# Performance work log

Measured on AMD Instinct MI355X. Metric: run time of the kernel, lower is better.

Reference implementation:

```python
import jax, jax.numpy as jnp
import numpy as np

EPS_BN = 1e-5
CLAMP_MAX = 1e-10  # nn.Hardtanh(min_val=0, max_val=1e-10) on squared dists


def _three_nn(xyz1, xyz2):
    # xyz1: (b, n, 3), xyz2: (b, m, 3) -> sq dists (b, n, 3), idx (b, n, 3)
    d2 = (jnp.sum(xyz1 ** 2, -1, keepdims=True)
          - 2.0 * jnp.einsum('bnc,bmc->bnm', xyz1, xyz2)
          + jnp.sum(xyz2 ** 2, -1)[:, None, :])  # (b, n, m)
    neg, idx = jax.lax.top_k(-d2, 3)
    return -neg, idx


def _conv_bn_relu(x, W, b, g, beta):
    # x: (b, n, cin); 1x1 Conv2d == pointwise linear, BN over (batch, spatial)
    y = jnp.einsum('bnc,oc->bno', x, W) + b
    mean = jnp.mean(y, axis=(0, 1))
    var = jnp.mean((y - mean) ** 2, axis=(0, 1))
    y = (y - mean) * jax.lax.rsqrt(var + EPS_BN) * g + beta
    return jax.nn.relu(y)


def setup_inputs() -> dict:
    key = jax.random.key(0)
    ks = jax.random.split(key, 8)
    b, n, m, c1, c2 = 16, 4096, 1024, 256, 512
    mlp, dimin = [256, 256], [c1 + c2, 256]
    inp = {
        'xyz1': jax.random.normal(ks[0], (b, n, 3), jnp.float32),
        'xyz2': jax.random.normal(ks[1], (b, m, 3), jnp.float32),
        'points1': jax.random.normal(ks[2], (b, n, c1), jnp.float32),
        'points2': jax.random.normal(ks[3], (b, m, c2), jnp.float32),
        'W1': jax.random.normal(ks[4], (mlp[0], dimin[0]), jnp.float32) * 0.02,
        'b1': jnp.zeros((mlp[0],), jnp.float32),
        'g1': jnp.ones((mlp[0],), jnp.float32),
        'beta1': jnp.zeros((mlp[0],), jnp.float32),
        'W2': jax.random.normal(ks[5], (mlp[1], dimin[1]), jnp.float32) * 0.02,
        'b2': jnp.zeros((mlp[1],), jnp.float32),
        'g2': jnp.ones((mlp[1],), jnp.float32),
        'beta2': jnp.zeros((mlp[1],), jnp.float32),
    }
    return inp


def reference(xyz1, xyz2, points1, points2, W1, b1, g1, beta1, W2, b2, g2, beta2):
    dist, idx = _three_nn(xyz1, xyz2)                     # (b, n, 3)
    dist = jnp.clip(dist, 0.0, CLAMP_MAX)                 # Hardtanh(0, 1e-10)
    inv = 1.0 / dist
    weight = inv / jnp.sum(inv, axis=2, keepdims=True)    # (b, n, 3)
    neigh = jax.vmap(lambda p, i: p[i])(points2, idx)     # (b, n, 3, c2)
    interp = jnp.einsum('bnk,bnkc->bnc', weight, neigh)   # (b, n, c2)
    feat = jnp.concatenate([interp, points1], axis=2)     # (b, n, c2+c1)
    feat = _conv_bn_relu(feat, W1, b1, g1, beta1)
    feat = _conv_bn_relu(feat, W2, b2, g2, beta2)
    return jnp.transpose(feat, (0, 2, 1))                 # (b, c_out, n)
```

## Files before the change

### kernel.cpp

```cpp
#include <hip/hip_runtime.h>

typedef unsigned short u16;
typedef short sh8 __attribute__((ext_vector_type(8)));
typedef float floatx4 __attribute__((ext_vector_type(4)));
typedef float float4v __attribute__((ext_vector_type(4)));
typedef u16 us8 __attribute__((ext_vector_type(8)));
typedef u16 us4 __attribute__((ext_vector_type(4)));

#define NB    16
#define NPTS  4096
#define MPTS  1024
#define CC1   256
#define CC2   512
#define KK1   768
#define CCO   256
#define MT    (NB*NPTS)
#define MZ    (NB*MPTS)

__device__ __forceinline__ float b2f(u16 u) {
    union { unsigned i; float f; } v; v.i = ((unsigned)u) << 16; return v.f;
}
__device__ __forceinline__ u16 f2b(float f) {
    union { float f; unsigned i; } v; v.f = f;
    unsigned u = v.i;
    unsigned r = (u + 0x7fffu + ((u >> 16) & 1u)) >> 16;
    return (u16)r;
}
__device__ __forceinline__ float ldv(const void* p, size_t i, int f32) {
    return f32 ? ((const float*)p)[i] : b2f(((const u16*)p)[i]);
}
__device__ __forceinline__ void stv(void* p, size_t i, int f32, float v) {
    if (f32) ((float*)p)[i] = v; else ((u16*)p)[i] = f2b(v);
}
__device__ __forceinline__ void gl_lds16(const void* g, void* l) {
    __builtin_amdgcn_global_load_lds(
        (const __attribute__((address_space(1))) void*)g,
        (__attribute__((address_space(3))) void*)l, 16, 0, 0);
}

__global__ void Pointnet_fp_module_33071248179394_kernel(
        const unsigned* g1bits, int* flag, float* stats) {
    int i = blockIdx.x * 256 + threadIdx.x;
    stats[i] = 0.f;
    if (i == 0) flag[0] = (g1bits[0] == 0x3F800000u) ? 1 : 0;
}

__global__ __launch_bounds__(512) void three_nn_k(
        const int* flagp, const void* xyz1, const void* xyz2,
        int* nidx, float* nw) {
    __shared__ float4 P[MPTS];
    __shared__ float md[512][3];
    __shared__ int   mi[512][3];
    const int f32 = flagp[0];
    const int bi = blockIdx.x >> 6;
    const int chunk = blockIdx.x & 63;
    const int t = threadIdx.x;
    const int ql = t & 63, sp = t >> 6;

    for (int p = t; p < MPTS; p += 512) {
        size_t s = (size_t)(bi * MPTS + p) * 3;
        P[p] = make_float4(ldv(xyz2, s, f32), ldv(xyz2, s + 1, f32),
                           ldv(xyz2, s + 2, f32), 0.f);
    }
    __syncthreads();

    const int q = chunk * 64 + ql;
    size_t s1 = (size_t)(bi * NPTS + q) * 3;
    const float qx = ldv(xyz1, s1 + 0, f32);
    const float qy = ldv(xyz1, s1 + 1, f32);
    const float qz = ldv(xyz1, s1 + 2, f32);

    float d0 = 3e38f, d1 = 3e38f, dv2 = 3e38f;
    int i0 = -1, i1 = -1, i2 = -1;
    const int jbeg = sp * 128, jend = jbeg + 128;
    #pragma unroll 4
    for (int j = jbeg; j < jend; j++) {
        float4 p = P[j];
        float dx = qx - p.x;
        float dy = qy - p.y;
        float dz = qz - p.z;
        float dd = fmaf(dx, dx, fmaf(dy, dy, dz * dz));
        if (dd < dv2) {
            if (dd < d0)      { dv2 = d1; i2 = i1; d1 = d0; i1 = i0; d0 = dd; i0 = j; }
            else if (dd < d1) { dv2 = d1; i2 = i1; d1 = dd; i1 = j; }
            else              { dv2 = dd; i2 = j; }
        }
    }
    md[t][0] = d0;  md[t][1] = d1;  md[t][2] = dv2;
    mi[t][0] = i0;  mi[t][1] = i1;  mi[t][2] = i2;
    __syncthreads();

    if (t < 64) {
        float b0 = 3e38f, b1 = 3e38f, b2v = 3e38f;
        int j0 = -1, j1 = -1, j2 = -1;
        #pragma unroll
        for (int s = 0; s < 8; s++) {
            int base = s * 64 + t;
            #pragma unroll
            for (int k = 0; k < 3; k++) {
                float d = md[base][k];
                int ji = mi[base][k];
                if (d < b0)      { b2v = b1; j2 = j1; b1 = b0; j1 = j0; b0 = d; j0 = ji; }
                else if (d < b1) { b2v = b1; j2 = j1; b1 = d; j1 = ji; }
                else if (d < b2v){ b2v = d; j2 = ji; }
            }
        }
        float e0 = fminf(fmaxf(b0, 0.f), 1e-10f);
        float e1 = fminf(fmaxf(b1, 0.f), 1e-10f);
        float e2 = fminf(fmaxf(b2v, 0.f), 1e-10f);
        float v0 = 1.0f / e0, v1 = 1.0f / e1, v2 = 1.0f / e2;
        float s = v0 + v1 + v2;
        const size_t gq = ((size_t)bi * NPTS + chunk * 64 + t) * 3;
        nidx[gq + 0] = j0; nidx[gq + 1] = j1; nidx[gq + 2] = j2;
        nw[gq + 0] = v0 / s; nw[gq + 1] = v1 / s; nw[gq + 2] = v2 / s;
    }
}

__global__ __launch_bounds__(256) void cvt_w_k(
        const int* flagp, const void* W1, const void* W2,
        u16* Wa, u16* Wbp, u16* W2b) {
    const int f32 = flagp[0];
    const int i = blockIdx.x * 256 + threadIdx.x;
    if (i < CCO * CC2) {
        int r = i >> 9, c = i & 511;
        Wa[i] = f2b(ldv(W1, (size_t)r * KK1 + c, f32));
    } else if (i < CCO * CC2 + CCO * CC1) {
        int k = i - CCO * CC2;
        int r = k >> 8, c = k & 255;
        Wbp[k] = f2b(ldv(W1, (size_t)r * KK1 + CC2 + c, f32));
    } else {
        int k = i - CCO * CC2 - CCO * CC1;
        W2b[k] = f2b(ldv(W2, k, f32));
    }
}

__global__ __launch_bounds__(256) void cvt_pts_k(
        const int* flagp, const void* p2, const void* p1,
        u16* p2b, u16* p1b) {
    const int f32 = flagp[0];
    size_t i = ((size_t)blockIdx.x * 256 + threadIdx.x) * 8;
    const size_t N2 = (size_t)MZ * CC2;
    const void* src; u16* dst; size_t off;
    if (i < N2) { src = p2; dst = p2b; off = i; }
    else        { src = p1; dst = p1b; off = i - N2; }
    us8 o;
    if (f32) {
        float4v a = *(const float4v*)((const float*)src + off);
        float4v b = *(const float4v*)((const float*)src + off + 4);
        #pragma unroll
        for (int k = 0; k < 4; k++) { o[k] = f2b(a[k]); o[k + 4] = f2b(b[k]); }
    } else {
        o = *(const us8*)((const u16*)src + off);
    }
    *(us8*)(dst + off) = o;
}

template<int K, bool STATS>
__global__ __launch_bounds__(256, 2) void gemm_bt(
        const int* flagp, const u16* __restrict__ A, const u16* __restrict__ B,
        const void* __restrict__ bias, u16* __restrict__ Y,
        float* __restrict__ sum, float* __restrict__ sq) {
    __shared__ u16 As[128 * 32];
    __shared__ u16 Bs[128 * 32];
    __shared__ float sSum[128], sSq[128];
    const int f32 = flagp[0];
    const int tid = threadIdx.x;
    const int m0 = blockIdx.x * 128;
    const int n0 = blockIdx.y * 128;
    const int wave = tid >> 6, lane = tid & 63;
    const int wm = wave & 1, wn = wave >> 1;
    const int l16 = lane & 15, quad = lane >> 4;

    if (STATS && tid < 128) { sSum[tid] = 0.f; sSq[tid] = 0.f; }

    floatx4 acc[4][4];
    #pragma unroll
    for (int i = 0; i < 4; i++)
        #pragma unroll
        for (int j = 0; j < 4; j++)
            acc[i][j] = (floatx4){0.f, 0.f, 0.f, 0.f};

    for (int kb = 0; kb < K; kb += 32) {
        __syncthreads();
        #pragma unroll
        for (int tt = 0; tt < 2; tt++) {
            int chunk = tid + tt * 256;
            int row = chunk >> 2, c4 = chunk & 3;
            gl_lds16(A + (size_t)(m0 + row) * K + kb + c4 * 8, As + chunk * 8);
            gl_lds16(B + (size_t)(n0 + row) * K + kb + c4 * 8, Bs + chunk * 8);
        }
        __syncthreads();

        sh8 af[4], bfr[4];
        #pragma unroll
        for (int i = 0; i < 4; i++)
            af[i] = *(const sh8*)(As + (wm * 64 + i * 16 + l16) * 32 + quad * 8);
        #pragma unroll
        for (int j = 0; j < 4; j++)
            bfr[j] = *(const sh8*)(Bs + (wn * 64 + j * 16 + l16) * 32 + quad * 8);
        #pragma unroll
        for (int i = 0; i < 4; i++)
            #pragma unroll
            for (int j = 0; j < 4; j++)
                acc[i][j] = __builtin_amdgcn_mfma_f32_16x16x32_bf16(
                                bfr[j], af[i], acc[i][j], 0, 0, 0);
    }

    float bvv[4][4];
    #pragma unroll
    for (int j = 0; j < 4; j++)
        #pragma unroll
        for (int r = 0; r < 4; r++) {
            int col = n0 + wn * 64 + j * 16 + quad * 4 + r;
            bvv[j][r] = bias ? ldv(bias, col, f32) : 0.f;
        }

    float cs[4][4], css[4][4];
    if (STATS) {
        #pragma unroll
        for (int j = 0; j < 4; j++)
            #pragma unroll
            for (int r = 0; r < 4; r++) { cs[j][r] = 0.f; css[j][r] = 0.f; }
    }

    #pragma unroll
    for (int i = 0; i < 4; i++) {
        int row = m0 + wm * 64 + i * 16 + l16;
        #pragma unroll
        for (int j = 0; j < 4; j++) {
            int colb = wn * 64 + j * 16 + quad * 4;
            us4 o;
            #pragma unroll
            for (int r = 0; r < 4; r++) {
                float v = acc[i][j][r] + bvv[j][r];
                if (STATS) { cs[j][r] += v; css[j][r] += v * v; }
                o[r] = f2b(v);
            }
            *(us4*)(Y + (size_t)row * CCO + n0 + colb) = o;
        }
    }
    if (STATS) {
        #pragma unroll
        for (int j = 0; j < 4; j++)
            #pragma unroll
            for (int r = 0; r < 4; r++) {
                float a = cs[j][r], b = css[j][r];
                #pragma unroll
                for (int m = 1; m < 16; m <<= 1) {
                    a += __shfl_xor(a, m, 64);
                    b += __shfl_xor(b, m, 64);
                }
                if (l16 == 0) {
                    int cl = wn * 64 + j * 16 + quad * 4 + r;
                    atomicAdd(&sSum[cl], a);
                    atomicAdd(&sSq[cl], b);
                }
            }
        __syncthreads();
        if (tid < 128) {
            atomicAdd(&sum[n0 + tid], sSum[tid]);
            atomicAdd(&sq[n0 + tid], sSq[tid]);
        }
    }
}

__global__ __launch_bounds__(256, 2) void gemm_p_k(
        const int* flagp, const u16* __restrict__ A, const u16* __restrict__ B,
        const void* __restrict__ bias, const int* __restrict__ nidx,
        const float* __restrict__ nw, const u16* __restrict__ Z,
        u16* __restrict__ Y, float* __restrict__ sum, float* __restrict__ sq) {
    __shared__ u16 As[128 * 32];
    __shared__ u16 Bs[128 * 32];
    __shared__ int   sIdx[128 * 3];
    __shared__ float sW[128 * 3];
    __shared__ float sSum[128], sSq[128];
    const int f32 = flagp[0];
    const int tid = threadIdx.x;
    const int m0 = blockIdx.x * 128;
    const int n0 = blockIdx.y * 128;
    const int wave = tid >> 6, lane = tid & 63;
    const int wm = wave & 1, wn = wave >> 1;
    const int l16 = lane & 15, quad = lane >> 4;
    const int zbase = (m0 >> 12) << 10;

    if (tid < 128) {
        size_t q3 = (size_t)(m0 + tid) * 3;
        #pragma unroll
        for (int k = 0; k < 3; k++) {
            sIdx[tid * 3 + k] = nidx[q3 + k];
            sW[tid * 3 + k]   = nw[q3 + k];
        }
        sSum[tid] = 0.f; sSq[tid] = 0.f;
    }

    floatx4 acc[4][4];
    #pragma unroll
    for (int i = 0; i < 4; i++)
        #pragma unroll
        for (int j = 0; j < 4; j++)
            acc[i][j] = (floatx4){0.f, 0.f, 0.f, 0.f};

    constexpr int K = 256;
    for (int kb = 0; kb < K; kb += 32) {
        __syncthreads();
        #pragma unroll
        for (int tt = 0; tt < 2; tt++) {
            int chunk = tid + tt * 256;
            int row = chunk >> 2, c4 = chunk & 3;
            gl_lds16(A + (size_t)(m0 + row) * K + kb + c4 * 8, As + chunk * 8);
            gl_lds16(B + (size_t)(n0 + row) * K + kb + c4 * 8, Bs + chunk * 8);
        }
        __syncthreads();

        sh8 af[4], bfr[4];
        #pragma unroll
        for (int i = 0; i < 4; i++)
            af[i] = *(const sh8*)(As + (wm * 64 + i * 16 + l16) * 32 + quad * 8);
        #pragma unroll
        for (int j = 0; j < 4; j++)
            bfr[j] = *(const sh8*)(Bs + (wn * 64 + j * 16 + l16) * 32 + quad * 8);
        #pragma unroll
        for (int i = 0; i < 4; i++)
            #pragma unroll
            for (int j = 0; j < 4; j++)
                acc[i][j] = __builtin_amdgcn_mfma_f32_16x16x32_bf16(
                                bfr[j], af[i], acc[i][j], 0, 0, 0);
    }

    float bvv[4][4];
    #pragma unroll
    for (int j = 0; j < 4; j++)
        #pragma unroll
        for (int r = 0; r < 4; r++)
            bvv[j][r] = ldv(bias, n0 + wn * 64 + j * 16 + quad * 4 + r, f32);

    float cs[4][4], css[4][4];
    #pragma unroll
    for (int j = 0; j < 4; j++)
        #pragma unroll
        for (int r = 0; r < 4; r++) { cs[j][r] = 0.f; css[j][r] = 0.f; }

    #pragma unroll
    for (int i = 0; i < 4; i++) {
        int rl = wm * 64 + i * 16 + l16;
        int i0 = sIdx[rl * 3 + 0], i1 = sIdx[rl * 3 + 1], i2 = sIdx[rl * 3 + 2];
        float w0 = sW[rl * 3 + 0], w1 = sW[rl * 3 + 1], w2 = sW[rl * 3 + 2];
        const u16* z0 = Z + (size_t)(zbase + i0) * CCO + n0;
        const u16* z1 = Z + (size_t)(zbase + i1) * CCO + n0;
        const u16* z2 = Z + (size_t)(zbase + i2) * CCO + n0;
        u16* yrow = Y + (size_t)(m0 + rl) * CCO + n0;
        #pragma unroll
        for (int j = 0; j < 4; j++) {
            int colb = wn * 64 + j * 16 + quad * 4;
            us4 zv0 = *(const us4*)(z0 + colb);
            us4 zv1 = *(const us4*)(z1 + colb);
            us4 zv2 = *(const us4*)(z2 + colb);
            us4 o;
            #pragma unroll
            for (int r = 0; r < 4; r++) {
                float v = acc[i][j][r] + bvv[j][r]
                        + w0 * b2f((u16)zv0[r]) + w1 * b2f((u16)zv1[r])
                        + w2 * b2f((u16)zv2[r]);
                cs[j][r] += v; css[j][r] += v * v;
                o[r] = f2b(v);
            }
            *(us4*)(yrow + colb) = o;
        }
    }
    #pragma unroll
    for (int j = 0; j < 4; j++)
        #pragma unroll
        for (int r = 0; r < 4; r++) {
            float a = cs[j][r], b = css[j][r];
            #pragma unroll
            for (int m = 1; m < 16; m <<= 1) {
                a += __shfl_xor(a, m, 64);
                b += __shfl_xor(b, m, 64);
            }
            if (l16 == 0) {
                int cl = wn * 64 + j * 16 + quad * 4 + r;
                atomicAdd(&sSum[cl], a);
                atomicAdd(&sSq[cl], b);
            }
        }
    __syncthreads();
    if (tid < 128) {
        atomicAdd(&sum[n0 + tid], sSum[tid]);
        atomicAdd(&sq[n0 + tid], sSq[tid]);
    }
}

__global__ __launch_bounds__(256) void bn_apply_k(
        const int* flagp, u16* Y, const float* sum, const float* sq,
        const void* g, const void* beta) {
    __shared__ float ssc[CCO], ssh[CCO];
    const int f32 = flagp[0];
    const int t = threadIdx.x;
    {
        const float invM = 1.0f / (float)MT;
        float mean = sum[t] * invM;
        float var = sq[t] * invM - mean * mean;
        float sc = rsqrtf(var + 1e-5f) * ldv(g, t, f32);
        ssc[t] = sc;
        ssh[t] = ldv(beta, t, f32) - mean * sc;
    }
    __syncthreads();
    const size_t base = ((size_t)blockIdx.x * 256 + t) * 16;
    const int c0 = (int)(base & (CCO - 1));
    us8 a = *(const us8*)(Y + base);
    us8 b = *(const us8*)(Y + base + 8);
    us8 oa, ob;
    #pragma unroll
    for (int k = 0; k < 8; k++) {
        oa[k] = f2b(fmaxf(b2f((u16)a[k]) * ssc[c0 + k] + ssh[c0 + k], 0.f));
        ob[k] = f2b(fmaxf(b2f((u16)b[k]) * ssc[c0 + 8 + k] + ssh[c0 + 8 + k], 0.f));
    }
    *(us8*)(Y + base) = oa;
    *(us8*)(Y + base + 8) = ob;
}

__global__ void bn_out_k(const int* flagp, const u16* Y, void* Out,
                         const float* sum, const float* sq,
                         const void* g, const void* beta) {
    __shared__ float tile[64][65];
    const int f32 = flagp[0];
    const int bi = blockIdx.z;
    const int p0 = blockIdx.x * 64;
    const int c0 = blockIdx.y * 64;
    const int t = threadIdx.x;
    const int cr = t & 63, rq = t >> 6;
    const float invM = 1.0f / (float)MT;

    const int c = c0 + cr;
    float mean = sum[c] * invM;
    float var = sq[c] * invM - mean * mean;
    float sc = rsqrtf(var + 1e-5f) * ldv(g, c, f32);
    float sh = ldv(beta, c, f32) - mean * sc;

    for (int r = rq; r < 64; r += 4) {
        int m = bi * NPTS + p0 + r;
        float v = b2f(Y[(size_t)m * CCO + c]) * sc + sh;
        tile[r][cr] = fmaxf(v, 0.f);
    }
    __syncthreads();
    for (int r = rq; r < 64; r += 4) {
        size_t o = ((size_t)bi * CCO + (c0 + r)) * NPTS + p0 + cr;
        stv(Out, o, f32, tile[cr][r]);
    }
}

extern "C" void kernel_launch(void* const* d_in, const int* in_sizes, int n_in,
                              void* d_out, int out_size, void* d_ws, size_t ws_size,
                              hipStream_t stream) {
    const void* xyz1    = d_in[0];
    const void* xyz2    = d_in[1];
    const void* points1 = d_in[2];
    const void* points2 = d_in[3];
    const void* W1      = d_in[4];
    const void* b1      = d_in[5];
    const void* g1      = d_in[6];
    const void* be1     = d_in[7];
    const void* W2      = d_in[8];
    const void* b2      = d_in[9];
    const void* g2      = d_in[10];
    const void* be2     = d_in[11];
    char* ws = (char*)d_ws;

    int*   flag  = (int*)(ws + 0);
    float* sum1  = (float*)(ws + 4096);
    float* sq1   = (float*)(ws + 5120);
    float* sum2  = (float*)(ws + 6144);
    float* sq2   = (float*)(ws + 7168);
    int*   nidx  = (int*)(ws + 20480);
    float* nw    = (float*)(ws + 806912);
    u16* Wa   = (u16*)(ws + 2097152);
    u16* Wbp  = (u16*)(ws + 2359296);
    u16* W2b  = (u16*)(ws + 2490368);
    u16* Z    = (u16*)(ws + 2621440);
    u16* p2b  = (u16*)(ws + 11010048ULL);
    u16* p1b  = (u16*)(ws + 27787264ULL);
    u16* y1   = (u16*)(ws + 61341696ULL);
    u16* y2   = (u16*)(ws + 94896128ULL);

    Pointnet_fp_module_33071248179394_kernel<<<dim3(16), dim3(256), 0, stream>>>(
        (const unsigned*)g1, flag, (float*)(ws + 4096));
    cvt_w_k<<<dim3(1024), dim3(256), 0, stream>>>(
        flag, W1, W2, Wa, Wbp, W2b);
    cvt_pts_k<<<dim3((MZ * CC2 + MT * CC1) / 2048), dim3(256), 0, stream>>>(
        flag, points2, points1, p2b, p1b);
    three_nn_k<<<dim3(1024), dim3(512), 0, stream>>>(flag, xyz1, xyz2, nidx, nw);
    gemm_bt<CC2, false><<<dim3(MZ / 128, CCO / 128), dim3(256), 0, stream>>>(
        flag, p2b, Wa, nullptr, Z, nullptr, nullptr);
    gemm_p_k<<<dim3(MT / 128, CCO / 128), dim3(256), 0, stream>>>(
        flag, p1b, Wbp, b1, nidx, nw, Z, y1, sum1, sq1);
    bn_apply_k<<<dim3(MT * CCO / 4096), dim3(256), 0, stream>>>(
        flag, y1, sum1, sq1, g1, be1);
    gemm_bt<CCO, true><<<dim3(MT / 128, CCO / 128), dim3(256), 0, stream>>>(
        flag, y1, W2b, b2, y2, sum2, sq2);
    bn_out_k<<<dim3(64, 4, NB), dim3(256), 0, stream>>>(
        flag, y2, d_out, sum2, sq2, g2, be2);
}
```

Before: 329.9 us.

## Fuse BN1 apply into second GEMM A-load and widen GEMM tiles to full N

Removes the standalone bn_apply kernel by applying the first BatchNorm scale/shift and ReLU while loading A tiles in the second GEMM, computing the per-channel scale/shift in shared memory. gemm_p_k and the second GEMM now use 512-thread blocks covering all 256 output channels, so each A tile is loaded once instead of twice. This saves a full read/write pass over y1 and halves A traffic. In exchange, the fused A load goes through registers instead of direct global-to-LDS copies, which adds latency to the un-pipelined K loop.

```diff
diff --git a/kernel.cpp b/kernel.cpp
--- a/kernel.cpp
+++ b/kernel.cpp
@@ -155,23 +155,36 @@
     *(us8*)(dst + off) = o;
 }
 
-template<int K, bool STATS>
-__global__ __launch_bounds__(256, 2) void gemm_bt(
+template<int K, int NW, bool STATS, bool BN1>
+__global__ __launch_bounds__(128 * NW, 2) void gemm_bt(
         const int* flagp, const u16* __restrict__ A, const u16* __restrict__ B,
         const void* __restrict__ bias, u16* __restrict__ Y,
-        float* __restrict__ sum, float* __restrict__ sq) {
+        float* __restrict__ sum, float* __restrict__ sq,
+        const float* __restrict__ nsum, const float* __restrict__ nsq,
+        const void* __restrict__ ng, const void* __restrict__ nbeta) {
+    constexpr int T  = 128 * NW;
+    constexpr int NT = NW * 64;
     __shared__ u16 As[128 * 32];
-    __shared__ u16 Bs[128 * 32];
-    __shared__ float sSum[128], sSq[128];
+    __shared__ u16 Bs[NT * 32];
+    __shared__ float sSum[STATS ? NT : 1], sSq[STATS ? NT : 1];
+    __shared__ float ssc[BN1 ? 256 : 1], ssh[BN1 ? 256 : 1];
     const int f32 = flagp[0];
     const int tid = threadIdx.x;
     const int m0 = blockIdx.x * 128;
-    const int n0 = blockIdx.y * 128;
+    const int n0 = blockIdx.y * NT;
     const int wave = tid >> 6, lane = tid & 63;
     const int wm = wave & 1, wn = wave >> 1;
     const int l16 = lane & 15, quad = lane >> 4;
 
-    if (STATS && tid < 128) { sSum[tid] = 0.f; sSq[tid] = 0.f; }
+    if (STATS && tid < NT) { sSum[tid] = 0.f; sSq[tid] = 0.f; }
+    if (BN1 && tid < 256) {
+        const float invM = 1.0f / (float)MT;
+        float mean = nsum[tid] * invM;
+        float var = nsq[tid] * invM - mean * mean;
+        float sc = rsqrtf(var + 1e-5f) * ldv(ng, tid, f32);
+        ssc[tid] = sc;
+        ssh[tid] = ldv(nbeta, tid, f32) - mean * sc;
+    }
 
     floatx4 acc[4][4];
     #pragma unroll
@@ -183,11 +196,25 @@
     for (int kb = 0; kb < K; kb += 32) {
         __syncthreads();
         #pragma unroll
-        for (int tt = 0; tt < 2; tt++) {
-            int chunk = tid + tt * 256;
-            int row = chunk >> 2, c4 = chunk & 3;
-            gl_lds16(A + (size_t)(m0 + row) * K + kb + c4 * 8, As + chunk * 8);
-            gl_lds16(B + (size_t)(n0 + row) * K + kb + c4 * 8, Bs + chunk * 8);
+        for (int c = tid; c < 512; c += T) {
+            int row = c >> 2, c4 = c & 3;
+            if (BN1) {
+                us8 a = *(const us8*)(A + (size_t)(m0 + row) * K + kb + c4 * 8);
+                us8 o;
+                #pragma unroll
+                for (int k = 0; k < 8; k++) {
+                    int ch = kb + c4 * 8 + k;
+                    o[k] = f2b(fmaxf(b2f((u16)a[k]) * ssc[ch] + ssh[ch], 0.f));
+                }
+                *(us8*)(As + c * 8) = o;
+            } else {
+                gl_lds16(A + (size_t)(m0 + row) * K + kb + c4 * 8, As + c * 8);
+            }
+        }
+        #pragma unroll
+        for (int c = tid; c < NT * 4; c += T) {
+            int row = c >> 2, c4 = c & 3;
+            gl_lds16(B + (size_t)(n0 + row) * K + kb + c4 * 8, Bs + c * 8);
         }
         __syncthreads();
 
@@ -257,27 +284,26 @@
                 }
             }
         __syncthreads();
-        if (tid < 128) {
+        if (tid < NT) {
             atomicAdd(&sum[n0 + tid], sSum[tid]);
             atomicAdd(&sq[n0 + tid], sSq[tid]);
         }
     }
 }
 
-__global__ __launch_bounds__(256, 2) void gemm_p_k(
+__global__ __launch_bounds__(512, 2) void gemm_p_k(
         const int* flagp, const u16* __restrict__ A, const u16* __restrict__ B,
         const void* __restrict__ bias, const int* __restrict__ nidx,
         const float* __restrict__ nw, const u16* __restrict__ Z,
         u16* __restrict__ Y, float* __restrict__ sum, float* __restrict__ sq) {
     __shared__ u16 As[128 * 32];
-    __shared__ u16 Bs[128 * 32];
+    __shared__ u16 Bs[256 * 32];
     __shared__ int   sIdx[128 * 3];
     __shared__ float sW[128 * 3];
-    __shared__ float sSum[128], sSq[128];
+    __shared__ float sSum[256], sSq[256];
     const int f32 = flagp[0];
     const int tid = threadIdx.x;
     const int m0 = blockIdx.x * 128;
-    const int n0 = blockIdx.y * 128;
     const int wave = tid >> 6, lane = tid & 63;
     const int wm = wave & 1, wn = wave >> 1;
     const int l16 = lane & 15, quad = lane >> 4;
@@ -290,8 +316,8 @@
             sIdx[tid * 3 + k] = nidx[q3 + k];
             sW[tid * 3 + k]   = nw[q3 + k];
         }
-        sSum[tid] = 0.f; sSq[tid] = 0.f;
-    }
+    }
+    if (tid < 256) { sSum[tid] = 0.f; sSq[tid] = 0.f; }
 
     floatx4 acc[4][4];
     #pragma unroll
@@ -303,12 +329,14 @@
     constexpr int K = 256;
     for (int kb = 0; kb < K; kb += 32) {
         __syncthreads();
-        #pragma unroll
-        for (int tt = 0; tt < 2; tt++) {
-            int chunk = tid + tt * 256;
-            int row = chunk >> 2, c4 = chunk & 3;
-            gl_lds16(A + (size_t)(m0 + row) * K + kb + c4 * 8, As + chunk * 8);
-            gl_lds16(B + (size_t)(n0 + row) * K + kb + c4 * 8, Bs + chunk * 8);
+        {
+            int row = tid >> 2, c4 = tid & 3;
+            gl_lds16(A + (size_t)(m0 + row) * K + kb + c4 * 8, As + tid * 8);
+        }
+        #pragma unroll
+        for (int c = tid; c < 1024; c += 512) {
+            int row = c >> 2, c4 = c & 3;
+            gl_lds16(B + (size_t)row * K + kb + c4 * 8, Bs + c * 8);
         }
         __syncthreads();
 
@@ -332,7 +360,7 @@
     for (int j = 0; j < 4; j++)
         #pragma unroll
         for (int r = 0; r < 4; r++)
-            bvv[j][r] = ldv(bias, n0 + wn * 64 + j * 16 + quad * 4 + r, f32);
+            bvv[j][r] = ldv(bias, wn * 64 + j * 16 + quad * 4 + r, f32);
 
     float cs[4][4], css[4][4];
     #pragma unroll
@@ -345,10 +373,10 @@
         int rl = wm * 64 + i * 16 + l16;
         int i0 = sIdx[rl * 3 + 0], i1 = sIdx[rl * 3 + 1], i2 = sIdx[rl * 3 + 2];
         float w0 = sW[rl * 3 + 0], w1 = sW[rl * 3 + 1], w2 = sW[rl * 3 + 2];
-        const u16* z0 = Z + (size_t)(zbase + i0) * CCO + n0;
-        const u16* z1 = Z + (size_t)(zbase + i1) * CCO + n0;
-        const u16* z2 = Z + (size_t)(zbase + i2) * CCO + n0;
-        u16* yrow = Y + (size_t)(m0 + rl) * CCO + n0;
+        const u16* z0 = Z + (size_t)(zbase + i0) * CCO;
+        const u16* z1 = Z + (size_t)(zbase + i1) * CCO;
+        const u16* z2 = Z + (size_t)(zbase + i2) * CCO;
+        u16* yrow = Y + (size_t)(m0 + rl) * CCO;
         #pragma unroll
         for (int j = 0; j < 4; j++) {
             int colb = wn * 64 + j * 16 + quad * 4;
@@ -384,39 +412,10 @@
             }
         }
     __syncthreads();
-    if (tid < 128) {
-        atomicAdd(&sum[n0 + tid], sSum[tid]);
-        atomicAdd(&sq[n0 + tid], sSq[tid]);
-    }
-}
-
-__global__ __launch_bounds__(256) void bn_apply_k(
-        const int* flagp, u16* Y, const float* sum, const float* sq,
-        const void* g, const void* beta) {
-    __shared__ float ssc[CCO], ssh[CCO];
-    const int f32 = flagp[0];
-    const int t = threadIdx.x;
-    {
-        const float invM = 1.0f / (float)MT;
-        float mean = sum[t] * invM;
-        float var = sq[t] * invM - mean * mean;
-        float sc = rsqrtf(var + 1e-5f) * ldv(g, t, f32);
-        ssc[t] = sc;
-        ssh[t] = ldv(beta, t, f32) - mean * sc;
-    }
-    __syncthreads();
-    const size_t base = ((size_t)blockIdx.x * 256 + t) * 16;
-    const int c0 = (int)(base & (CCO - 1));
-    us8 a = *(const us8*)(Y + base);
-    us8 b = *(const us8*)(Y + base + 8);
-    us8 oa, ob;
-    #pragma unroll
-    for (int k = 0; k < 8; k++) {
-        oa[k] = f2b(fmaxf(b2f((u16)a[k]) * ssc[c0 + k] + ssh[c0 + k], 0.f));
-        ob[k] = f2b(fmaxf(b2f((u16)b[k]) * ssc[c0 + 8 + k] + ssh[c0 + 8 + k], 0.f));
-    }
-    *(us8*)(Y + base) = oa;
-    *(us8*)(Y + base + 8) = ob;
+    if (tid < 256) {
+        atomicAdd(&sum[tid], sSum[tid]);
+        atomicAdd(&sq[tid], sSq[tid]);
+    }
 }
 
 __global__ void bn_out_k(const int* flagp, const u16* Y, void* Out,
@@ -489,14 +488,14 @@
     cvt_pts_k<<<dim3((MZ * CC2 + MT * CC1) / 2048), dim3(256), 0, stream>>>(
         flag, points2, points1, p2b, p1b);
     three_nn_k<<<dim3(1024), dim3(512), 0, stream>>>(flag, xyz1, xyz2, nidx, nw);
-    gemm_bt<CC2, false><<<dim3(MZ / 128, CCO / 128), dim3(256), 0, stream>>>(
-        flag, p2b, Wa, nullptr, Z, nullptr, nullptr);
-    gemm_p_k<<<dim3(MT / 128, CCO / 128), dim3(256), 0, stream>>>(
+    gemm_bt<CC2, 2, false, false><<<dim3(MZ / 128, 2), dim3(256), 0, stream>>>(
+        flag, p2b, Wa, nullptr, Z, nullptr, nullptr,
+        nullptr, nullptr, nullptr, nullptr);
+    gemm_p_k<<<dim3(MT / 128), dim3(512), 0, stream>>>(
         flag, p1b, Wbp, b1, nidx, nw, Z, y1, sum1, sq1);
-    bn_apply_k<<<dim3(MT * CCO / 4096), dim3(256), 0, stream>>>(
-        flag, y1, sum1, sq1, g1, be1);
-    gemm_bt<CCO, true><<<dim3(MT / 128, CCO / 128), dim3(256), 0, stream>>>(
-        flag, y1, W2b, b2, y2, sum2, sq2);
+    gemm_bt<CCO, 4, true, true><<<dim3(MT / 128, 1), dim3(512), 0, stream>>>(
+        flag, y1, W2b, b2, y2, sum2, sq2,
+        sum1, sq1, g1, be1);
     bn_out_k<<<dim3(64, 4, NB), dim3(256), 0, stream>>>(
         flag, y2, d_out, sum2, sq2, g2, be2);
 }
```

Result: no change. 324.5 us (-1.6%).
